# Kernel tuning notes

Measured on AMD Instinct MI355X. Metric: run time of the kernel, lower is better.

## Reference

```python
import jax, jax.numpy as jnp
import numpy as np

C_Z = 128
C_HIDDEN = 32
N_HEAD = 4
HC = N_HEAD * C_HIDDEN  # 128
LN_EPS = 1e-5


def setup_inputs() -> dict:
    key = jax.random.key(0)
    ks = jax.random.split(key, 8)
    b, n = 1, 256
    s = 1.0 / np.sqrt(C_Z)
    return {
        "z_ij": jax.random.normal(ks[0], (b, n, n, C_Z), dtype=jnp.float32),
        "ln_gamma": jnp.ones((C_Z,), dtype=jnp.float32),
        "ln_beta": jnp.zeros((C_Z,), dtype=jnp.float32),
        "Wq": jax.random.normal(ks[1], (C_Z, HC), dtype=jnp.float32) * s,
        "Wk": jax.random.normal(ks[2], (C_Z, HC), dtype=jnp.float32) * s,
        "Wv": jax.random.normal(ks[3], (C_Z, HC), dtype=jnp.float32) * s,
        "Wb": jax.random.normal(ks[4], (C_Z, N_HEAD), dtype=jnp.float32) * s,
        "Wg": jax.random.normal(ks[5], (C_Z, HC), dtype=jnp.float32) * s,
        "Wout": jax.random.normal(ks[6], (HC, C_Z), dtype=jnp.float32) * (1.0 / np.sqrt(HC)),
    }


def reference(z_ij, ln_gamma, ln_beta, Wq, Wk, Wv, Wb, Wg, Wout):
    b, n, _, _ = z_ij.shape
    # LayerNorm over c_z
    mu = jnp.mean(z_ij, axis=-1, keepdims=True)
    var = jnp.var(z_ij, axis=-1, keepdims=True)
    z = (z_ij - mu) * jax.lax.rsqrt(var + LN_EPS) * ln_gamma + ln_beta

    def heads(x):  # [b,i,j,hc] -> [b,i,j,h,d]
        return x.reshape(b, n, n, N_HEAD, C_HIDDEN)

    q = heads(z @ Wq)
    k = heads(z @ Wk)
    v = heads(z @ Wv)
    bias = z @ Wb                      # [b,i,j,h]
    g = jax.nn.sigmoid(heads(z @ Wg))  # [b,i,j,h,d]

    scores = jnp.einsum('bijhd,bikhd->bijkh', q, k) / np.sqrt(C_HIDDEN)
    scores = scores + bias[:, None]    # bias[b, j, k, h] broadcast over i
    a = jax.nn.softmax(scores, axis=-2)  # over k
    o = jnp.einsum('bijkh,bikhd->bijhd', a, v)
    o = (g * o).reshape(b, n, n, HC)
    return o @ Wout
```

## Files before the change

### kernel.cpp

```cpp
#include <hip/hip_runtime.h>

typedef _Float16 f16x8 __attribute__((ext_vector_type(8)));
typedef _Float16 f16x2 __attribute__((ext_vector_type(2)));
typedef float f32x4 __attribute__((ext_vector_type(4)));

#define MFMA16(a, b, c) __builtin_amdgcn_mfma_f32_16x16x32_f16(a, b, c, 0, 0, 0)

#define NROW 65536
#define SEGB 16777216ull
#define LOG2E 1.4426950408889634f

__global__ __launch_bounds__(256) void k_ln(
    const float* __restrict__ z, const float* __restrict__ gamma,
    const float* __restrict__ beta, const float* __restrict__ Wb,
    const float* __restrict__ Wq, const float* __restrict__ Wk,
    const float* __restrict__ Wv, const float* __restrict__ Wg,
    const float* __restrict__ Wout,
    _Float16* __restrict__ zln, float* __restrict__ biasT,
    _Float16* __restrict__ WtAll)
{
  __shared__ _Float16 sw[32 * 136];
  int bid = blockIdx.x;
  if (bid < 16384) {
    int lane = threadIdx.x & 63;
    int w = threadIdx.x >> 6;
    int row = bid * 4 + w;
    float2 v = ((const float2*)(z + (size_t)row * 128))[lane];
    float s = v.x + v.y;
    #pragma unroll
    for (int m = 1; m < 64; m <<= 1) s += __shfl_xor(s, m);
    float mu = s * 0.0078125f;
    float dx = v.x - mu, dy = v.y - mu;
    float q = dx * dx + dy * dy;
    #pragma unroll
    for (int m = 1; m < 64; m <<= 1) q += __shfl_xor(q, m);
    float rs = rsqrtf(q * 0.0078125f + 1e-5f);
    float2 g2 = ((const float2*)gamma)[lane];
    float2 b2 = ((const float2*)beta)[lane];
    float y0 = dx * rs * g2.x + b2.x;
    float y1 = dy * rs * g2.y + b2.y;
    f16x2 pr; pr.x = (_Float16)y0; pr.y = (_Float16)y1;
    *(f16x2*)(zln + (size_t)row * 128 + 2 * lane) = pr;
  } else if (bid < 16384 + 20) {
    int t = bid - 16384;
    int mat = t >> 2, n0 = (t & 3) * 32;
    const float* src = (mat == 0) ? Wq : (mat == 1) ? Wk : (mat == 2) ? Wv
                       : (mat == 3) ? Wg : Wout;
    _Float16* dst = WtAll + ((mat == 4) ? 5 : mat) * 16384;
    for (int it = 0; it < 16; ++it) {
      int e = threadIdx.x + it * 256;
      int c = e >> 5, j = e & 31;
      sw[j * 136 + c] = (_Float16)src[c * 128 + n0 + j];
    }
    __syncthreads();
    for (int it = 0; it < 2; ++it) {
      int ch = threadIdx.x + it * 256;
      int n = ch >> 4, k8 = (ch & 15) * 8;
      *(int4*)(dst + (n0 + n) * 128 + k8) = *(const int4*)&sw[n * 136 + k8];
    }
  } else {
    _Float16* dst = WtAll + 4 * 16384;
    for (int e = threadIdx.x; e < 16384; e += 256) {
      int n = e >> 7, k = e & 127;
      dst[e] = (n < 4) ? (_Float16)Wb[k * 4 + n] : (_Float16)0.f;
    }
  }
}

__global__ __launch_bounds__(256) void k_proj(
    const _Float16* __restrict__ A, const _Float16* __restrict__ WtAll,
    _Float16* __restrict__ Qb, _Float16* __restrict__ Kb,
    _Float16* __restrict__ Vb, _Float16* __restrict__ Gb,
    float* __restrict__ biasT)
{
  __shared__ _Float16 sA[128 * 136];
  __shared__ _Float16 sB[128 * 136];
  int e = blockIdx.x;
  int xcd = e & 7;
  int t = e >> 3;
  int by = t % 5;
  int g = t / 5;
  int m0 = (g * 8 + xcd) * 128;
  const _Float16* Bt = WtAll + by * 16384;
  _Float16* outp = (by == 0) ? Qb : (by == 1) ? Kb : (by == 2) ? Vb : Gb;
  int tid = threadIdx.x;
  for (int it = 0; it < 8; ++it) {
    int ch = tid + it * 256;
    int r = ch >> 4, c8 = (ch & 15) * 8;
    *(int4*)&sA[r * 136 + c8] = *(const int4*)(A + (size_t)(m0 + r) * 128 + c8);
    *(int4*)&sB[r * 136 + c8] = *(const int4*)(Bt + r * 128 + c8);
  }
  __syncthreads();
  int lane = tid & 63, w = tid >> 6;
  int mw = (w >> 1) * 64, nw = (w & 1) * 64;
  int lr = lane & 15, lg = lane >> 4;
  int ntm = (by == 4) ? 1 : 4;
  f32x4 z4 = {0.f, 0.f, 0.f, 0.f};
  f32x4 acc[4][4];
  #pragma unroll
  for (int mt = 0; mt < 4; ++mt)
    #pragma unroll
    for (int nt = 0; nt < 4; ++nt) acc[mt][nt] = z4;
  #pragma unroll
  for (int k0 = 0; k0 < 128; k0 += 32) {
    f16x8 af[4], bf[4];
    #pragma unroll
    for (int mt = 0; mt < 4; ++mt)
      af[mt] = *(const f16x8*)&sA[(mw + mt * 16 + lr) * 136 + k0 + lg * 8];
    #pragma unroll
    for (int nt = 0; nt < 4; ++nt)
      if (nt < ntm)
        bf[nt] = *(const f16x8*)&sB[(nw + nt * 16 + lr) * 136 + k0 + lg * 8];
    #pragma unroll
    for (int mt = 0; mt < 4; ++mt)
      #pragma unroll
      for (int nt = 0; nt < 4; ++nt)
        if (nt < ntm)
          acc[mt][nt] = MFMA16(af[mt], bf[nt], acc[mt][nt]);
  }
  if (by == 4) {
    if (nw == 0 && lr < 4) {
      #pragma unroll
      for (int mt = 0; mt < 4; ++mt)
        #pragma unroll
        for (int r = 0; r < 4; ++r) {
          int row = m0 + mw + mt * 16 + lg * 4 + r;
          int lowk = row & 255;
          int pos = (row & ~255) | ((lowk & 15) << 4) | (lowk >> 4);
          biasT[(size_t)lr * NROW + pos] = acc[mt][0][r] * LOG2E;
        }
    }
    return;
  }
  bool sig = (by == 3);
  #pragma unroll
  for (int mt = 0; mt < 4; ++mt)
    #pragma unroll
    for (int nt = 0; nt < 4; ++nt)
      #pragma unroll
      for (int r = 0; r < 4; ++r) {
        int row = m0 + mw + mt * 16 + lg * 4 + r;
        int col = nw + nt * 16 + lr;
        float v = acc[mt][nt][r];
        if (sig) v = 1.0f / (1.0f + __expf(-v));
        outp[(size_t)row * 128 + col] = (_Float16)v;
      }
}

__global__ __launch_bounds__(256) void k_attn(
    const _Float16* __restrict__ Qb, const _Float16* __restrict__ Kb,
    const _Float16* __restrict__ Vb, const _Float16* __restrict__ Gb,
    const float* __restrict__ biasT, _Float16* __restrict__ OG)
{
  __shared__ _Float16 sK[256 * 32];
  __shared__ _Float16 sV[32 * 256];
  __shared__ _Float16 sP[64 * 256];
  int i = blockIdx.x, h = blockIdx.y;
  int tid = threadIdx.x;
  size_t base = ((size_t)i * 256) * 128 + h * 32;
  for (int it = 0; it < 4; ++it) {
    int ch = tid + it * 256;
    int r = ch >> 2, cx = ch & 3;
    int p = cx ^ ((r >> 1) & 3);
    *(int4*)&sK[r * 32 + p * 8] = *(const int4*)(Kb + base + (size_t)r * 128 + cx * 8);
  }
  for (int it = 0; it < 4; ++it) {
    int ch = tid + it * 256;
    int k = ch >> 2, d8 = (ch & 3) * 8;
    f16x8 tv = *(const f16x8*)(Vb + base + (size_t)k * 128 + d8);
    int k2 = ((k & 15) << 4) | (k >> 4);
    int c2 = k2 >> 3, e2 = k2 & 7;
    #pragma unroll
    for (int jj = 0; jj < 8; ++jj) {
      int d = d8 + jj;
      int p = c2 ^ (d & 7);
      sV[d * 256 + p * 8 + e2] = tv[jj];
    }
  }
  __syncthreads();
  int lane = tid & 63, w = tid >> 6;
  int lr = lane & 15, lg = lane >> 4;
  const float scale = 0.2550348858f;
  f32x4 z4 = {0.f, 0.f, 0.f, 0.f};
  for (int pass = 0; pass < 4; ++pass) {
    int jbase = pass * 64;
    int jq = jbase + w * 16 + lr;
    f16x8 aq = *(const f16x8*)(Qb + base + (size_t)jq * 128 + lg * 8);
    f32x4 sacc[16];
    __builtin_amdgcn_s_setprio(1);
    #pragma unroll
    for (int kt = 0; kt < 16; ++kt) {
      int r = kt * 16 + lr;
      int p = lg ^ ((r >> 1) & 3);
      f16x8 bk = *(const f16x8*)&sK[r * 32 + p * 8];
      sacc[kt] = MFMA16(aq, bk, z4);
    }
    __builtin_amdgcn_s_setprio(0);
    float rinv4[4];
    #pragma unroll
    for (int r = 0; r < 4; ++r) {
      int j = jbase + w * 16 + lg * 4 + r;
      const float* brow = biasT + (size_t)h * NROW + (size_t)j * 256 + lr * 16;
      float4 b4[4];
      #pragma unroll
      for (int m = 0; m < 4; ++m) b4[m] = ((const float4*)brow)[m];
      float mx = -1e30f;
      #pragma unroll
      for (int kt = 0; kt < 16; ++kt) {
        float bb = ((const float*)&b4[kt >> 2])[kt & 3];
        float sv = sacc[kt][r] * scale + bb;
        sacc[kt][r] = sv;
        mx = fmaxf(mx, sv);
      }
      #pragma unroll
      for (int msk = 1; msk < 16; msk <<= 1) mx = fmaxf(mx, __shfl_xor(mx, msk));
      float sum = 0.f;
      f16x8 h0, h1;
      #pragma unroll
      for (int kt = 0; kt < 16; ++kt) {
        float pv = exp2f(sacc[kt][r] - mx);
        sum += pv;
        if (kt < 8) h0[kt] = (_Float16)pv;
        else        h1[kt - 8] = (_Float16)pv;
      }
      #pragma unroll
      for (int msk = 1; msk < 16; msk <<= 1) sum += __shfl_xor(sum, msk);
      rinv4[r] = 1.0f / sum;
      int row = w * 16 + lg * 4 + r;
      *(f16x8*)&sP[row * 256 + ((2 * lr) ^ (row & 7)) * 8] = h0;
      *(f16x8*)&sP[row * 256 + ((2 * lr + 1) ^ (row & 7)) * 8] = h1;
    }
    f32x4 oacc[2] = {z4, z4};
    int prow = w * 16 + lr;
    #pragma unroll
    for (int ks = 0; ks < 8; ++ks) {
      int c = ks * 4 + lg;
      f16x8 ap = *(const f16x8*)&sP[prow * 256 + (c ^ (prow & 7)) * 8];
      __builtin_amdgcn_s_setprio(1);
      #pragma unroll
      for (int nt = 0; nt < 2; ++nt) {
        int d = nt * 16 + lr;
        f16x8 bv = *(const f16x8*)&sV[d * 256 + (c ^ (d & 7)) * 8];
        oacc[nt] = MFMA16(ap, bv, oacc[nt]);
      }
      __builtin_amdgcn_s_setprio(0);
    }
    #pragma unroll
    for (int nt = 0; nt < 2; ++nt)
      #pragma unroll
      for (int r = 0; r < 4; ++r) {
        int j = jbase + w * 16 + lg * 4 + r;
        int d = nt * 16 + lr;
        size_t idx = base + (size_t)j * 128 + d;
        float g = (float)Gb[idx];
        OG[idx] = (_Float16)(oacc[nt][r] * rinv4[r] * g);
      }
  }
}

__global__ __launch_bounds__(256) void k_outp(
    const _Float16* __restrict__ A, const _Float16* __restrict__ Bt,
    float* __restrict__ out)
{
  __shared__ _Float16 sA[128 * 136];
  __shared__ _Float16 sB[128 * 136];
  int m0 = blockIdx.x * 128;
  int tid = threadIdx.x;
  for (int it = 0; it < 8; ++it) {
    int ch = tid + it * 256;
    int r = ch >> 4, c8 = (ch & 15) * 8;
    *(int4*)&sA[r * 136 + c8] = *(const int4*)(A + (size_t)(m0 + r) * 128 + c8);
    *(int4*)&sB[r * 136 + c8] = *(const int4*)(Bt + r * 128 + c8);
  }
  __syncthreads();
  int lane = tid & 63, w = tid >> 6;
  int mw = (w >> 1) * 64, nw = (w & 1) * 64;
  int lr = lane & 15, lg = lane >> 4;
  f32x4 z4 = {0.f, 0.f, 0.f, 0.f};
  f32x4 acc[4][4];
  #pragma unroll
  for (int mt = 0; mt < 4; ++mt)
    #pragma unroll
    for (int nt = 0; nt < 4; ++nt) acc[mt][nt] = z4;
  #pragma unroll
  for (int k0 = 0; k0 < 128; k0 += 32) {
    f16x8 af[4], bf[4];
    #pragma unroll
    for (int mt = 0; mt < 4; ++mt)
      af[mt] = *(const f16x8*)&sA[(mw + mt * 16 + lr) * 136 + k0 + lg * 8];
    #pragma unroll
    for (int nt = 0; nt < 4; ++nt)
      bf[nt] = *(const f16x8*)&sB[(nw + nt * 16 + lr) * 136 + k0 + lg * 8];
    #pragma unroll
    for (int mt = 0; mt < 4; ++mt)
      #pragma unroll
      for (int nt = 0; nt < 4; ++nt)
        acc[mt][nt] = MFMA16(af[mt], bf[nt], acc[mt][nt]);
  }
  #pragma unroll
  for (int mt = 0; mt < 4; ++mt)
    #pragma unroll
    for (int nt = 0; nt < 4; ++nt)
      #pragma unroll
      for (int r = 0; r < 4; ++r) {
        int row = m0 + mw + mt * 16 + lg * 4 + r;
        int col = nw + nt * 16 + lr;
        out[(size_t)row * 128 + col] = acc[mt][nt][r];
      }
}

extern "C" void kernel_launch(void* const* d_in, const int* in_sizes, int n_in,
                              void* d_out, int out_size, void* d_ws, size_t ws_size,
                              hipStream_t stream) {
  (void)in_sizes; (void)n_in; (void)out_size; (void)ws_size;
  const float* z    = (const float*)d_in[0];
  const float* gam  = (const float*)d_in[1];
  const float* bet  = (const float*)d_in[2];
  const float* Wq   = (const float*)d_in[3];
  const float* Wk   = (const float*)d_in[4];
  const float* Wv   = (const float*)d_in[5];
  const float* Wb   = (const float*)d_in[6];
  const float* Wg   = (const float*)d_in[7];
  const float* Wout = (const float*)d_in[8];

  char* ws = (char*)d_ws;
  _Float16* zln   = (_Float16*)(ws);
  _Float16* Qb    = (_Float16*)(ws + SEGB);
  _Float16* Kb    = (_Float16*)(ws + SEGB * 2);
  _Float16* Vb    = (_Float16*)(ws + SEGB * 3);
  _Float16* Gb    = (_Float16*)(ws + SEGB * 4);
  float*    biasT = (float*)   (ws + SEGB * 5);
  _Float16* WtAll = (_Float16*)(ws + SEGB * 5 + 1048576);

  k_ln<<<16405, 256, 0, stream>>>(z, gam, bet, Wb, Wq, Wk, Wv, Wg, Wout,
                                  zln, biasT, WtAll);
  k_proj<<<2560, 256, 0, stream>>>(zln, WtAll, Qb, Kb, Vb, Gb, biasT);
  k_attn<<<dim3(256, 4), 256, 0, stream>>>(Qb, Kb, Vb, Gb, biasT, zln);
  k_outp<<<512, 256, 0, stream>>>(zln, WtAll + 5 * 16384, (float*)d_out);
}
```

Baseline: 192.0 us.

## Fuse LayerNorm into projection kernel, computing normalized tile in shared memory

Removes the standalone LayerNorm pass and its fp16 intermediate buffer. Each projection block now reads raw fp32 rows of z, computes mean and variance with a single-pass sum and sum-of-squares split across two threads per row, and writes the normalized fp16 tile straight into shared memory. The weight-conversion work moves into a small separate kernel. In exchange, LayerNorm is recomputed five times per row tile (once per output projection), fp32 input traffic is repeated, and the E[x^2]-mu^2 variance form is less numerically robust.

```diff
diff --git a/kernel.cpp b/kernel.cpp
--- a/kernel.cpp
+++ b/kernel.cpp
@@ -1,6 +1,7 @@
 #include <hip/hip_runtime.h>
 
 typedef _Float16 f16x8 __attribute__((ext_vector_type(8)));
+typedef _Float16 f16x4 __attribute__((ext_vector_type(4)));
 typedef _Float16 f16x2 __attribute__((ext_vector_type(2)));
 typedef float f32x4 __attribute__((ext_vector_type(4)));
 
@@ -10,40 +11,16 @@
 #define SEGB 16777216ull
 #define LOG2E 1.4426950408889634f
 
-__global__ __launch_bounds__(256) void k_ln(
-    const float* __restrict__ z, const float* __restrict__ gamma,
-    const float* __restrict__ beta, const float* __restrict__ Wb,
-    const float* __restrict__ Wq, const float* __restrict__ Wk,
-    const float* __restrict__ Wv, const float* __restrict__ Wg,
-    const float* __restrict__ Wout,
-    _Float16* __restrict__ zln, float* __restrict__ biasT,
+__global__ __launch_bounds__(256) void k_wt(
+    const float* __restrict__ Wb, const float* __restrict__ Wq,
+    const float* __restrict__ Wk, const float* __restrict__ Wv,
+    const float* __restrict__ Wg, const float* __restrict__ Wout,
     _Float16* __restrict__ WtAll)
 {
   __shared__ _Float16 sw[32 * 136];
   int bid = blockIdx.x;
-  if (bid < 16384) {
-    int lane = threadIdx.x & 63;
-    int w = threadIdx.x >> 6;
-    int row = bid * 4 + w;
-    float2 v = ((const float2*)(z + (size_t)row * 128))[lane];
-    float s = v.x + v.y;
-    #pragma unroll
-    for (int m = 1; m < 64; m <<= 1) s += __shfl_xor(s, m);
-    float mu = s * 0.0078125f;
-    float dx = v.x - mu, dy = v.y - mu;
-    float q = dx * dx + dy * dy;
-    #pragma unroll
-    for (int m = 1; m < 64; m <<= 1) q += __shfl_xor(q, m);
-    float rs = rsqrtf(q * 0.0078125f + 1e-5f);
-    float2 g2 = ((const float2*)gamma)[lane];
-    float2 b2 = ((const float2*)beta)[lane];
-    float y0 = dx * rs * g2.x + b2.x;
-    float y1 = dy * rs * g2.y + b2.y;
-    f16x2 pr; pr.x = (_Float16)y0; pr.y = (_Float16)y1;
-    *(f16x2*)(zln + (size_t)row * 128 + 2 * lane) = pr;
-  } else if (bid < 16384 + 20) {
-    int t = bid - 16384;
-    int mat = t >> 2, n0 = (t & 3) * 32;
+  if (bid < 20) {
+    int mat = bid >> 2, n0 = (bid & 3) * 32;
     const float* src = (mat == 0) ? Wq : (mat == 1) ? Wk : (mat == 2) ? Wv
                        : (mat == 3) ? Wg : Wout;
     _Float16* dst = WtAll + ((mat == 4) ? 5 : mat) * 16384;
@@ -68,7 +45,8 @@
 }
 
 __global__ __launch_bounds__(256) void k_proj(
-    const _Float16* __restrict__ A, const _Float16* __restrict__ WtAll,
+    const float* __restrict__ z, const float* __restrict__ gamma,
+    const float* __restrict__ beta, const _Float16* __restrict__ WtAll,
     _Float16* __restrict__ Qb, _Float16* __restrict__ Kb,
     _Float16* __restrict__ Vb, _Float16* __restrict__ Gb,
     float* __restrict__ biasT)
@@ -87,8 +65,35 @@
   for (int it = 0; it < 8; ++it) {
     int ch = tid + it * 256;
     int r = ch >> 4, c8 = (ch & 15) * 8;
-    *(int4*)&sA[r * 136 + c8] = *(const int4*)(A + (size_t)(m0 + r) * 128 + c8);
     *(int4*)&sB[r * 136 + c8] = *(const int4*)(Bt + r * 128 + c8);
+  }
+  {
+    int row = tid >> 1, half = tid & 1;
+    const float* zr = z + (size_t)(m0 + row) * 128 + half * 64;
+    float4 v[16];
+    float s = 0.f, s2 = 0.f;
+    #pragma unroll
+    for (int q = 0; q < 16; ++q) {
+      v[q] = ((const float4*)zr)[q];
+      s  += (v[q].x + v[q].y) + (v[q].z + v[q].w);
+      s2 += (v[q].x * v[q].x + v[q].y * v[q].y)
+          + (v[q].z * v[q].z + v[q].w * v[q].w);
+    }
+    s += __shfl_xor(s, 1);
+    s2 += __shfl_xor(s2, 1);
+    float mu = s * 0.0078125f;
+    float rs = rsqrtf(fmaxf(s2 * 0.0078125f - mu * mu, 0.f) + 1e-5f);
+    #pragma unroll
+    for (int q = 0; q < 16; ++q) {
+      float4 g4 = ((const float4*)gamma)[half * 16 + q];
+      float4 b4 = ((const float4*)beta)[half * 16 + q];
+      f16x4 o;
+      o.x = (_Float16)((v[q].x - mu) * rs * g4.x + b4.x);
+      o.y = (_Float16)((v[q].y - mu) * rs * g4.y + b4.y);
+      o.z = (_Float16)((v[q].z - mu) * rs * g4.z + b4.z);
+      o.w = (_Float16)((v[q].w - mu) * rs * g4.w + b4.w);
+      *(f16x4*)&sA[row * 136 + half * 64 + q * 4] = o;
+    }
   }
   __syncthreads();
   int lane = tid & 63, w = tid >> 6;
@@ -324,7 +329,7 @@
   const float* Wout = (const float*)d_in[8];
 
   char* ws = (char*)d_ws;
-  _Float16* zln   = (_Float16*)(ws);
+  _Float16* OG    = (_Float16*)(ws);
   _Float16* Qb    = (_Float16*)(ws + SEGB);
   _Float16* Kb    = (_Float16*)(ws + SEGB * 2);
   _Float16* Vb    = (_Float16*)(ws + SEGB * 3);
@@ -332,9 +337,8 @@
   float*    biasT = (float*)   (ws + SEGB * 5);
   _Float16* WtAll = (_Float16*)(ws + SEGB * 5 + 1048576);
 
-  k_ln<<<16405, 256, 0, stream>>>(z, gam, bet, Wb, Wq, Wk, Wv, Wg, Wout,
-                                  zln, biasT, WtAll);
-  k_proj<<<2560, 256, 0, stream>>>(zln, WtAll, Qb, Kb, Vb, Gb, biasT);
-  k_attn<<<dim3(256, 4), 256, 0, stream>>>(Qb, Kb, Vb, Gb, biasT, zln);
-  k_outp<<<512, 256, 0, stream>>>(zln, WtAll + 5 * 16384, (float*)d_out);
-}
+  k_wt<<<21, 256, 0, stream>>>(Wb, Wq, Wk, Wv, Wg, Wout, WtAll);
+  k_proj<<<2560, 256, 0, stream>>>(z, gam, bet, WtAll, Qb, Kb, Vb, Gb, biasT);
+  k_attn<<<dim3(256, 4), 256, 0, stream>>>(Qb, Kb, Vb, Gb, biasT, OG);
+  k_outp<<<512, 256, 0, stream>>>(OG, WtAll + 5 * 16384, (float*)d_out);
+}
```

New measurement: 234.3 us. 1.22x slower.
